# Performance work log

Measured on AMD Instinct MI355X. Metric: run time of the kernel, lower is better.

Reference implementation:

```python
import jax, jax.numpy as jnp
import numpy as np

B, C, H, W = 1, 128, 48, 48
HC = 32                     # head_channel
NH = C // HC                # num heads = 4
K = 16                      # n_clusters
N = H * W                   # 2304
SCALE = HC ** 0.5
EPS = 1e-6


def setup_inputs() -> dict:
    key = jax.random.key(0)
    ks = jax.random.split(key, 20)
    s = 0.05  # weight init scale ~ xavier-ish for C=128
    def g(i, shape, sc=s):
        return jax.random.normal(ks[i], shape, dtype=jnp.float32) * sc
    return {
        'q_img': g(0, (B, C, H, W), 1.0),
        'k_img_map': g(1, (B, C, H, W), 1.0),
        'v_img_map': g(2, (B, C, H, W), 1.0),
        'pixel_coefficients': jax.random.uniform(ks[3], (B, N, N), dtype=jnp.float32),
        'labels': jax.random.randint(ks[4], (B, H, W), 0, K),
        # projections (stored as [in, out]; y = x @ w + b)
        'wq': g(5, (C, C)), 'bq': jnp.zeros((C,), jnp.float32),
        'wk': g(6, (C, C)), 'bk': jnp.zeros((C,), jnp.float32),
        'wv': g(7, (C, C)), 'bv': jnp.zeros((C,), jnp.float32),
        # mlp_1: Linear(C,2C) -> LeakyReLU(0.01) -> Linear(2C,C) (dropout=0 -> identity)
        'w1a': g(8, (C, 2 * C)), 'b1a': jnp.zeros((2 * C,), jnp.float32),
        'w1b': g(9, (2 * C, C)), 'b1b': jnp.zeros((C,), jnp.float32),
        # mlp_2
        'w2a': g(10, (C, 2 * C)), 'b2a': jnp.zeros((2 * C,), jnp.float32),
        'w2b': g(11, (2 * C, C)), 'b2b': jnp.zeros((C,), jnp.float32),
    }


def _mlp(x, wa, ba, wb, bb):
    h = x @ wa + ba
    h = jax.nn.leaky_relu(h, negative_slope=0.01)
    return h @ wb + bb


def reference(q_img, k_img_map, v_img_map, pixel_coefficients,
              wq, bq, wk, bk, wv, bv,
              w1a, b1a, w1b, b1b, w2a, b2a, w2b, b2b,
              labels):
    # projections on channel-last pixels
    q = q_img.transpose(0, 2, 3, 1).reshape(B, N, C) @ wq + bq
    k = k_img_map.transpose(0, 2, 3, 1).reshape(B, N, C) @ wk + bk
    v = v_img_map.transpose(0, 2, 3, 1).reshape(B, N, C) @ wv + bv

    labels_flat = labels.reshape(B, N)
    onehot = jax.nn.one_hot(labels_flat, K, dtype=q.dtype)        # [B,N,K]
    num_k = jnp.einsum('bnk,bnc->bkc', onehot, k)                 # [B,K,C]
    den_k = onehot.sum(axis=1)[:, :, None] + EPS                  # [B,K,1]
    centers_k = num_k / den_k

    qm = q.reshape(B, N, NH, HC).transpose(0, 2, 1, 3)            # [B,h,N,d]
    km = k.reshape(B, N, NH, HC).transpose(0, 2, 1, 3)
    vm = v.reshape(B, N, NH, HC).transpose(0, 2, 1, 3)
    kcm = centers_k.reshape(B, K, NH, HC).transpose(0, 2, 1, 3)   # [B,h,K,d]

    attn_intra = jnp.einsum('bhid,bhjd->bhij', qm, km)            # [B,h,N,N]
    attn_centers = jnp.einsum('bhid,bhkd->bhik', qm, kcm)         # [B,h,N,K]

    # gather center score per key's cluster: attn_centers[b,h,i,labels[b,j]]
    idx = jnp.broadcast_to(labels_flat[:, None, None, :], (B, NH, N, N))
    attn_inter = jnp.take_along_axis(attn_centers, idx, axis=3)   # [B,h,N,N]
    attn_inter = attn_inter * pixel_coefficients[:, None, :, :]

    same = labels_flat[:, None, :, None] == labels_flat[:, None, None, :]  # [B,1,N,N]
    scores = jnp.where(same, attn_intra, attn_inter) / SCALE
    attn_w = jax.nn.softmax(scores, axis=-1)

    out = jnp.einsum('bhij,bhjd->bhid', attn_w, vm)
    out = out.transpose(0, 2, 1, 3).reshape(B, N, C)              # [B,N,C]

    v_spatial = v.reshape(B, H, W, C).transpose(0, 3, 1, 2)       # [B,C,H,W]
    rs1 = v_spatial + _mlp(out, w1a, b1a, w1b, b1b).transpose(0, 2, 1).reshape(B, C, H, W)
    rs1_flat = rs1.transpose(0, 2, 3, 1).reshape(B, N, C)
    rs2 = rs1 + _mlp(rs1_flat, w2a, b2a, w2b, b2b).transpose(0, 2, 1).reshape(B, C, H, W)
    return rs2
```

## Files before the change

### kernel.cpp

```cpp
#include <hip/hip_runtime.h>
#include <hip/hip_bf16.h>
#include <math.h>

#define NPIX 2304
#define CCH  128
#define NH   4
#define HC   32
#define NCL  16
#define KSPLIT 8
#define KEYS 288
#define NSTEP 9
#define QSCALE 0.25503489f
#define PPT  16

typedef __attribute__((ext_vector_type(8))) short short8;
typedef __attribute__((ext_vector_type(4))) float f32x4;

#if __has_builtin(__builtin_amdgcn_exp2f)
#define EXP2(x) __builtin_amdgcn_exp2f(x)
#else
#define EXP2(x) __expf((x) * 0.6931471805599453f)
#endif

static __device__ __forceinline__ short f2bf(float x) {
    __hip_bfloat16 b = __float2bfloat16(x);
    return *reinterpret_cast<short*>(&b);
}

__global__ void __launch_bounds__(256) pack_w_kernel(
        const float* __restrict__ w1a, const float* __restrict__ w1b,
        const float* __restrict__ w2a, const float* __restrict__ w2b,
        const float* __restrict__ wq,  const float* __restrict__ wk,
        const float* __restrict__ wv,
        float4* __restrict__ p1a, float4* __restrict__ p1b,
        float4* __restrict__ p2a, float4* __restrict__ p2b,
        float4* __restrict__ pq,  float4* __restrict__ pk,
        float4* __restrict__ pv) {
    const int idx = blockIdx.x * 256 + threadIdx.x;
    const float* src; float4* dst; int sh, local;
    if (idx < 8192)       { src = w1a; dst = p1a; sh = 8; local = idx; }
    else if (idx < 16384) { src = w1b; dst = p1b; sh = 7; local = idx - 8192; }
    else if (idx < 24576) { src = w2a; dst = p2a; sh = 8; local = idx - 16384; }
    else if (idx < 32768) { src = w2b; dst = p2b; sh = 7; local = idx - 24576; }
    else if (idx < 36864) { src = wq;  dst = pq;  sh = 7; local = idx - 32768; }
    else if (idx < 40960) { src = wk;  dst = pk;  sh = 7; local = idx - 36864; }
    else                  { src = wv;  dst = pv;  sh = 7; local = idx - 40960; }
    const int OUT = 1 << sh;
    const int g = local >> sh, o = local & (OUT - 1);
    float4 v;
    v.x = src[(4 * g + 0) * OUT + o];
    v.y = src[(4 * g + 1) * OUT + o];
    v.z = src[(4 * g + 2) * OUT + o];
    v.w = src[(4 * g + 3) * OUT + o];
    dst[local] = v;
}

__global__ void __launch_bounds__(256) proj_kernel(
        const float* __restrict__ xq, const float* __restrict__ xk,
        const float* __restrict__ xv, const int* __restrict__ labels,
        const float4* __restrict__ pq, const float* __restrict__ bq,
        const float4* __restrict__ pk, const float* __restrict__ bk,
        const float4* __restrict__ pv, const float* __restrict__ bv,
        short* __restrict__ qbf, short* __restrict__ kbf,
        float* __restrict__ vbuf, short* __restrict__ vbfT,
        float* __restrict__ cpart, float* __restrict__ denpart) {
    __shared__ float xsP[CCH * PPT];
    __shared__ float ls2[2 * NCL * CCH];
    __shared__ float smls[32];
    const int which = blockIdx.y;
    const int pxblk = blockIdx.x;
    const int n0    = pxblk * PPT;
    const int t  = threadIdx.x;
    const int c  = t & 127;
    const int ph = t >> 7;
    const float*  x  = (which == 0) ? xq : (which == 1) ? xk : xv;
    const float4* wp = (which == 0) ? pq : (which == 1) ? pk : pv;
    const float*  b  = (which == 0) ? bq : (which == 1) ? bk : bv;

#pragma unroll
    for (int it = 0; it < 8; ++it) {
        const int flat = it * 256 + t;
        const int cc = flat >> 4;
        const int p  = flat & 15;
        xsP[flat] = x[cc * NPIX + n0 + p];
    }
    if (which == 1)
        for (int u = t; u < 2 * NCL * CCH; u += 256) ls2[u] = 0.f;
    __syncthreads();

    float acc[8];
    const float bb = b[c];
#pragma unroll
    for (int p = 0; p < 8; ++p) acc[p] = bb;

    for (int g = 0; g < CCH / 4; ++g) {
        const float4 w4 = wp[g * 128 + c];
#pragma unroll
        for (int j = 0; j < 4; ++j) {
            const float wv_ = (j == 0) ? w4.x : (j == 1) ? w4.y : (j == 2) ? w4.z : w4.w;
            const float4 xa = *(const float4*)(xsP + (4 * g + j) * PPT + ph * 8);
            const float4 xb = *(const float4*)(xsP + (4 * g + j) * PPT + ph * 8 + 4);
            acc[0] = fmaf(xa.x, wv_, acc[0]); acc[1] = fmaf(xa.y, wv_, acc[1]);
            acc[2] = fmaf(xa.z, wv_, acc[2]); acc[3] = fmaf(xa.w, wv_, acc[3]);
            acc[4] = fmaf(xb.x, wv_, acc[4]); acc[5] = fmaf(xb.y, wv_, acc[5]);
            acc[6] = fmaf(xb.z, wv_, acc[6]); acc[7] = fmaf(xb.w, wv_, acc[7]);
        }
    }

    const int nb = n0 + ph * 8;
    if (which == 0) {
#pragma unroll
        for (int p = 0; p < 8; ++p)
            qbf[(size_t)(nb + p) * CCH + c] = f2bf(acc[p] * QSCALE);
    } else if (which == 1) {
#pragma unroll
        for (int p = 0; p < 8; ++p)
            kbf[(size_t)(nb + p) * CCH + c] = f2bf(acc[p]);
        int lab8[8];
#pragma unroll
        for (int p = 0; p < 8; ++p) lab8[p] = labels[nb + p];
#pragma unroll
        for (int p = 0; p < 8; ++p)
            ls2[(ph * NCL + lab8[p]) * CCH + c] += acc[p];
        if (t < 32) {
            const int g2 = t >> 4, cl = t & 15;
            int cnt = 0;
#pragma unroll
            for (int p = 0; p < 8; ++p)
                cnt += (labels[n0 + g2 * 8 + p] == cl) ? 1 : 0;
            smls[t] = (float)cnt;
        }
        __syncthreads();
        for (int u = t; u < NCL * CCH; u += 256)
            cpart[(size_t)pxblk * 2048 + u] = ls2[u] + ls2[2048 + u];
        if (t < 16)
            denpart[pxblk * 16 + t] = smls[t] + smls[16 + t];
    } else {
#pragma unroll
        for (int p = 0; p < 8; ++p) vbuf[(size_t)(nb + p) * CCH + c] = acc[p];
        short8 s0;
#pragma unroll
        for (int p = 0; p < 8; ++p) s0[p] = f2bf(acc[p]);
        *(short8*)(vbfT + (size_t)c * NPIX + nb) = s0;
    }
}

__global__ void centersB_kernel(const float* __restrict__ cpart,
                                const float* __restrict__ denpart,
                                short* __restrict__ cbf) {
    const int idx = blockIdx.x * 256 + threadIdx.x;
    const int kk  = idx >> 7;
    float den = 0.f, s = 0.f;
    for (int b = 0; b < 144; ++b) den += denpart[b * 16 + kk];
    for (int b = 0; b < 144; ++b) s   += cpart[(size_t)b * 2048 + idx];
    cbf[idx] = f2bf(s / (den + 1e-6f));
}

__global__ void __launch_bounds__(256, 4) attn_part_kernel(
        const short* __restrict__ qbf,  const short* __restrict__ kbf,
        const short* __restrict__ vbfT, const short* __restrict__ cbf,
        const int* __restrict__ labels, const float* __restrict__ pc,
        float* __restrict__ part_o, float* __restrict__ part_l) {
    __shared__ __align__(16) short Pl[NH][16 * 40];
    __shared__ __align__(16) float aclT[NH][16][16];
    __shared__ int   labl[KEYS];
    const int qt   = blockIdx.x;
    const int ks   = blockIdx.y;
    const int tid  = threadIdx.x;
    const int w    = tid >> 6;
    const int lane = tid & 63;
    const int quad = lane >> 4;
    const int lq   = lane & 15;
    const int i0   = qt * 16;
    const int j0   = ks * KEYS;

    for (int u = tid; u < KEYS / 4; u += 256)
        *(int4*)(labl + u * 4) = *(const int4*)(labels + j0 + u * 4);

    const short8 aq = *(const short8*)(qbf + (size_t)(i0 + lq) * CCH + w * HC + quad * 8);
    {
        const short8 bc = *(const short8*)(cbf + (size_t)lq * CCH + w * HC + quad * 8);
        f32x4 z = {0.f, 0.f, 0.f, 0.f};
        f32x4 acd = __builtin_amdgcn_mfma_f32_16x16x32_bf16(aq, bc, z, 0, 0, 0);
        *(f32x4*)(&aclT[w][lq][quad * 4]) = acd;
    }
    int labi[4];
#pragma unroll
    for (int r = 0; r < 4; ++r) labi[r] = labels[i0 + quad * 4 + r];

    __syncthreads();

    const short* kp  = kbf  + (size_t)(j0 + lq) * CCH + w * HC + quad * 8;
    const short* vp  = vbfT + (size_t)(w * HC + lq) * NPIX + j0 + quad * 8;
    const float* pcp = pc   + (size_t)(i0 + quad * 4) * NPIX + j0 + lq;

    short8 k0A, k1A, v0A, v1A, k0B, k1B, v0B, v1B;
    float pcA[8], pcB[8];
    f32x4 accO0 = {0.f, 0.f, 0.f, 0.f};
    f32x4 accO1 = {0.f, 0.f, 0.f, 0.f};
    float lp[4] = {0.f, 0.f, 0.f, 0.f};

#define ISSUE(K0_, K1_, V0_, V1_, s) do {                                         \
        K0_ = *(const short8*)(kp + (size_t)(s) * 32 * CCH);                      \
        K1_ = *(const short8*)(kp + (size_t)((s) * 32 + 16) * CCH);               \
        V0_ = *(const short8*)(vp + (s) * 32);                                    \
        V1_ = *(const short8*)(vp + (size_t)16 * NPIX + (s) * 32);                \
    } while (0)

#define ISSUE_PC(dst, s) do {                                                     \
        _Pragma("unroll")                                                         \
        for (int r_ = 0; r_ < 4; ++r_) {                                          \
            dst[r_ * 2 + 0] = pcp[(size_t)r_ * NPIX + (s) * 32];                  \
            dst[r_ * 2 + 1] = pcp[(size_t)r_ * NPIX + (s) * 32 + 16];             \
        }                                                                         \
    } while (0)

#define COMPUTE(s, K0_, K1_, V0_, V1_, PCUSE) do {                                \
        _Pragma("unroll")                                                         \
        for (int kh = 0; kh < 2; ++kh) {                                          \
            const short8 bk = (kh == 0) ? K0_ : K1_;                              \
            f32x4 z = {0.f, 0.f, 0.f, 0.f};                                       \
            const f32x4 sv = __builtin_amdgcn_mfma_f32_16x16x32_bf16(aq, bk, z, 0, 0, 0);\
            const int slab = labl[(s) * 32 + kh * 16 + lq];                       \
            const f32x4 av4 = *(const f32x4*)(&aclT[w][slab][quad * 4]);          \
            _Pragma("unroll")                                                     \
            for (int r = 0; r < 4; ++r) {                                         \
                const float sc_ = (slab == labi[r]) ? sv[r] : av4[r] * PCUSE[r * 2 + kh];\
                const float p   = EXP2(sc_);                                      \
                lp[r] += p;                                                       \
                Pl[w][(quad * 4 + r) * 40 + kh * 16 + lq] = f2bf(p);              \
            }                                                                     \
        }                                                                         \
        const short8 ap = *(const short8*)(&Pl[w][lq * 40 + quad * 8]);           \
        accO0 = __builtin_amdgcn_mfma_f32_16x16x32_bf16(ap, V0_, accO0, 0, 0, 0); \
        accO1 = __builtin_amdgcn_mfma_f32_16x16x32_bf16(ap, V1_, accO1, 0, 0, 0); \
    } while (0)

    ISSUE(k0A, k1A, v0A, v1A, 0);
    ISSUE_PC(pcA, 0);
    for (int sb = 0; sb < NSTEP; sb += 2) {
        if (sb + 1 < NSTEP) { ISSUE(k0B, k1B, v0B, v1B, sb + 1); ISSUE_PC(pcB, sb + 1); }
        COMPUTE(sb, k0A, k1A, v0A, v1A, pcA);
        if (sb + 1 < NSTEP) {
            if (sb + 2 < NSTEP) { ISSUE(k0A, k1A, v0A, v1A, sb + 2); ISSUE_PC(pcA, sb + 2); }
            COMPUTE(sb + 1, k0B, k1B, v0B, v1B, pcB);
        }
    }
#undef ISSUE
#undef ISSUE_PC
#undef COMPUTE

#pragma unroll
    for (int r = 0; r < 4; ++r) {
        float v = lp[r];
        v += __shfl_xor(v, 1, 64);
        v += __shfl_xor(v, 2, 64);
        v += __shfl_xor(v, 4, 64);
        v += __shfl_xor(v, 8, 64);
        lp[r] = v;
    }
    if (lq == 0) {
#pragma unroll
        for (int r = 0; r < 4; ++r)
            part_l[((size_t)ks * NPIX + i0 + quad * 4 + r) * NH + w] = lp[r];
    }
#pragma unroll
    for (int r = 0; r < 4; ++r) {
        float* po = part_o + ((size_t)ks * NPIX + i0 + quad * 4 + r) * CCH + w * HC;
        po[lq]      = accO0[r];
        po[16 + lq] = accO1[r];
    }
}

__global__ void __launch_bounds__(256) mlp_chain_kernel(
        const float* __restrict__ part_o, const float* __restrict__ part_l,
        const float* __restrict__ vbuf,
        const float4* __restrict__ p1a, const float* __restrict__ b1a,
        const float4* __restrict__ p1b, const float* __restrict__ b1b,
        const float4* __restrict__ p2a, const float* __restrict__ b2a,
        const float4* __restrict__ p2b, const float* __restrict__ b2b,
        float* __restrict__ outp) {
    __shared__ float xs[8 * CCH];
    __shared__ float hL[8 * 2 * CCH];
    __shared__ float r1L[8 * CCH];
    __shared__ float fT[CCH * 8];
    const int n0 = blockIdx.x * 8;
    const int t  = threadIdx.x;

    {
        const int p = t >> 5, c4 = (t & 31) * 4;
        const int hh2 = c4 >> 5;
        float ls_ = 0.f;
#pragma unroll
        for (int ks = 0; ks < KSPLIT; ++ks)
            ls_ += part_l[((size_t)ks * NPIX + n0 + p) * NH + hh2];
        float sx = 0.f, sy = 0.f, sz = 0.f, sw2 = 0.f;
#pragma unroll
        for (int ks = 0; ks < KSPLIT; ++ks) {
            const float4 v = *(const float4*)(part_o + ((size_t)ks * NPIX + n0 + p) * CCH + c4);
            sx += v.x; sy += v.y; sz += v.z; sw2 += v.w;
        }
        const float inv = 1.f / ls_;
        xs[p * CCH + c4 + 0] = sx * inv;
        xs[p * CCH + c4 + 1] = sy * inv;
        xs[p * CCH + c4 + 2] = sz * inv;
        xs[p * CCH + c4 + 3] = sw2 * inv;
    }
    __syncthreads();

    const int c  = t & 127;
    const int pg = t >> 7;

    {
        float ha[8];
        const float b1 = b1a[t];
#pragma unroll
        for (int p = 0; p < 8; ++p) ha[p] = b1;
        for (int g = 0; g < CCH / 4; ++g) {
            const float4 w4 = p1a[g * 2 * CCH + t];
#pragma unroll
            for (int p = 0; p < 8; ++p) {
                const float4 xv = *(const float4*)(xs + p * CCH + g * 4);
                ha[p] = fmaf(xv.x, w4.x, ha[p]); ha[p] = fmaf(xv.y, w4.y, ha[p]);
                ha[p] = fmaf(xv.z, w4.z, ha[p]); ha[p] = fmaf(xv.w, w4.w, ha[p]);
            }
        }
#pragma unroll
        for (int p = 0; p < 8; ++p) {
            const float v = ha[p];
            hL[p * 2 * CCH + t] = (v > 0.f) ? v : 0.01f * v;
        }
    }
    __syncthreads();

    {
        float oa[4];
        const float bo = b1b[c];
#pragma unroll
        for (int j = 0; j < 4; ++j) oa[j] = bo;
        for (int g = 0; g < 2 * CCH / 4; ++g) {
            const float4 w4 = p1b[g * CCH + c];
#pragma unroll
            for (int j = 0; j < 4; ++j) {
                const float4 hv = *(const float4*)(hL + (pg * 4 + j) * 2 * CCH + g * 4);
                oa[j] = fmaf(hv.x, w4.x, oa[j]); oa[j] = fmaf(hv.y, w4.y, oa[j]);
                oa[j] = fmaf(hv.z, w4.z, oa[j]); oa[j] = fmaf(hv.w, w4.w, oa[j]);
            }
        }
#pragma unroll
        for (int j = 0; j < 4; ++j)
            r1L[(pg * 4 + j) * CCH + c] =
                vbuf[(size_t)(n0 + pg * 4 + j) * CCH + c] + oa[j];
    }
    __syncthreads();

    {
        float ha[8];
        const float b2 = b2a[t];
#pragma unroll
        for (int p = 0; p < 8; ++p) ha[p] = b2;
        for (int g = 0; g < CCH / 4; ++g) {
            const float4 w4 = p2a[g * 2 * CCH + t];
#pragma unroll
            for (int p = 0; p < 8; ++p) {
                const float4 xv = *(const float4*)(r1L + p * CCH + g * 4);
                ha[p] = fmaf(xv.x, w4.x, ha[p]); ha[p] = fmaf(xv.y, w4.y, ha[p]);
                ha[p] = fmaf(xv.z, w4.z, ha[p]); ha[p] = fmaf(xv.w, w4.w, ha[p]);
            }
        }
        __syncthreads();
#pragma unroll
        for (int p = 0; p < 8; ++p) {
            const float v = ha[p];
            hL[p * 2 * CCH + t] = (v > 0.f) ? v : 0.01f * v;
        }
    }
    __syncthreads();

    {
        float oa[4];
        const float bo = b2b[c];
#pragma unroll
        for (int j = 0; j < 4; ++j) oa[j] = bo;
        for (int g = 0; g < 2 * CCH / 4; ++g) {
            const float4 w4 = p2b[g * CCH + c];
#pragma unroll
            for (int j = 0; j < 4; ++j) {
                const float4 hv = *(const float4*)(hL + (pg * 4 + j) * 2 * CCH + g * 4);
                oa[j] = fmaf(hv.x, w4.x, oa[j]); oa[j] = fmaf(hv.y, w4.y, oa[j]);
                oa[j] = fmaf(hv.z, w4.z, oa[j]); oa[j] = fmaf(hv.w, w4.w, oa[j]);
            }
        }
#pragma unroll
        for (int j = 0; j < 4; ++j)
            fT[c * 8 + pg * 4 + j] = r1L[(pg * 4 + j) * CCH + c] + oa[j];
    }
    __syncthreads();

    {
        const int cc = t >> 1, half = t & 1;
        const float4 v = *(const float4*)(fT + cc * 8 + half * 4);
        *(float4*)(outp + (size_t)cc * NPIX + n0 + half * 4) = v;
    }
}

extern "C" void kernel_launch(void* const* d_in, const int* in_sizes, int n_in,
                              void* d_out, int out_size, void* d_ws, size_t ws_size,
                              hipStream_t stream) {
    const float* q_img = (const float*)d_in[0];
    const float* k_img = (const float*)d_in[1];
    const float* v_img = (const float*)d_in[2];
    const float* pc    = (const float*)d_in[3];
    const int*   labels= (const int*)  d_in[4];
    const float* wq = (const float*)d_in[5];   const float* bq = (const float*)d_in[6];
    const float* wk = (const float*)d_in[7];   const float* bk = (const float*)d_in[8];
    const float* wv = (const float*)d_in[9];   const float* bv = (const float*)d_in[10];
    const float* w1a = (const float*)d_in[11]; const float* b1a = (const float*)d_in[12];
    const float* w1b = (const float*)d_in[13]; const float* b1b = (const float*)d_in[14];
    const float* w2a = (const float*)d_in[15]; const float* b2a = (const float*)d_in[16];
    const float* w2b = (const float*)d_in[17]; const float* b2b = (const float*)d_in[18];

    float* fw = (float*)d_ws;
    float* vbuf    = fw;
    float* part_o  = vbuf + (size_t)NPIX * CCH;
    float* part_l  = part_o + (size_t)KSPLIT * NPIX * CCH;
    float* cpart   = part_l + (size_t)KSPLIT * NPIX * NH;
    float* denpart = cpart + (size_t)144 * 2048;
    float* pkd     = denpart + 144 * 16;
    float4* p1a = (float4*)pkd;
    float4* p1b = p1a + 8192;
    float4* p2a = p1b + 8192;
    float4* p2b = p2a + 8192;
    float4* pq  = p2b + 8192;
    float4* pk4 = pq + 4096;
    float4* pv4 = pk4 + 4096;
    short* qbf     = (short*)(pv4 + 4096);
    short* kbf     = qbf + (size_t)NPIX * CCH;
    short* vbfT    = kbf + (size_t)NPIX * CCH;
    short* cbf     = vbfT + (size_t)NPIX * CCH;

    pack_w_kernel<<<176, 256, 0, stream>>>(
        w1a, w1b, w2a, w2b, wq, wk, wv, p1a, p1b, p2a, p2b, pq, pk4, pv4);
    proj_kernel<<<dim3(144, 3), 256, 0, stream>>>(
        q_img, k_img, v_img, labels, pq, bq, pk4, bk, pv4, bv,
        qbf, kbf, vbuf, vbfT, cpart, denpart);
    centersB_kernel<<<8, 256, 0, stream>>>(cpart, denpart, cbf);
    attn_part_kernel<<<dim3(144, KSPLIT), 256, 0, stream>>>(
        qbf, kbf, vbfT, cbf, labels, pc, part_o, part_l);
    mlp_chain_kernel<<<288, 256, 0, stream>>>(
        part_o, part_l, vbuf, p1a, b1a, p1b, b1b, p2a, b2a, p2b, b2b,
        (float*)d_out);
}
```

Before: 185.8 us.

## Run MLP chain on bf16 MFMA with transposed bf16 weight packing

Replaces the scalar-FMA fp32 MLP chain with bf16 MFMA 16x16x32 tiles, processing 16 pixels per block instead of 8. The pack kernel now emits transposed bf16 copies of the four MLP weight matrices laid out for MFMA B operands. Intermediate activations are staged in padded bf16 shared memory, while the residual is kept in fp32 registers. This cuts ALU time in the MLP stage, at the cost of bf16 rounding in the MLP inputs and weights and a halved block count.

```diff
diff --git a/kernel.cpp b/kernel.cpp
--- a/kernel.cpp
+++ b/kernel.cpp
@@ -14,6 +14,7 @@
 #define PPT  16
 
 typedef __attribute__((ext_vector_type(8))) short short8;
+typedef __attribute__((ext_vector_type(4))) short short4v;
 typedef __attribute__((ext_vector_type(4))) float f32x4;
 
 #if __has_builtin(__builtin_amdgcn_exp2f)
@@ -28,31 +29,46 @@
 }
 
 __global__ void __launch_bounds__(256) pack_w_kernel(
+        const float* __restrict__ wq,  const float* __restrict__ wk,
+        const float* __restrict__ wv,
         const float* __restrict__ w1a, const float* __restrict__ w1b,
         const float* __restrict__ w2a, const float* __restrict__ w2b,
-        const float* __restrict__ wq,  const float* __restrict__ wk,
-        const float* __restrict__ wv,
-        float4* __restrict__ p1a, float4* __restrict__ p1b,
-        float4* __restrict__ p2a, float4* __restrict__ p2b,
         float4* __restrict__ pq,  float4* __restrict__ pk,
-        float4* __restrict__ pv) {
+        float4* __restrict__ pv,
+        short* __restrict__ t1a, short* __restrict__ t1b,
+        short* __restrict__ t2a, short* __restrict__ t2b) {
     const int idx = blockIdx.x * 256 + threadIdx.x;
-    const float* src; float4* dst; int sh, local;
-    if (idx < 8192)       { src = w1a; dst = p1a; sh = 8; local = idx; }
-    else if (idx < 16384) { src = w1b; dst = p1b; sh = 7; local = idx - 8192; }
-    else if (idx < 24576) { src = w2a; dst = p2a; sh = 8; local = idx - 16384; }
-    else if (idx < 32768) { src = w2b; dst = p2b; sh = 7; local = idx - 24576; }
-    else if (idx < 36864) { src = wq;  dst = pq;  sh = 7; local = idx - 32768; }
-    else if (idx < 40960) { src = wk;  dst = pk;  sh = 7; local = idx - 36864; }
-    else                  { src = wv;  dst = pv;  sh = 7; local = idx - 40960; }
-    const int OUT = 1 << sh;
-    const int g = local >> sh, o = local & (OUT - 1);
-    float4 v;
-    v.x = src[(4 * g + 0) * OUT + o];
-    v.y = src[(4 * g + 1) * OUT + o];
-    v.z = src[(4 * g + 2) * OUT + o];
-    v.w = src[(4 * g + 3) * OUT + o];
-    dst[local] = v;
+    if (idx < 12288) {
+        const int which = idx >> 12, local = idx & 4095;
+        const float* src = (which == 0) ? wq : (which == 1) ? wk : wv;
+        float4*      dst = (which == 0) ? pq : (which == 1) ? pk : pv;
+        const int g = local >> 7, o = local & 127;
+        float4 v;
+        v.x = src[(4 * g + 0) * 128 + o];
+        v.y = src[(4 * g + 1) * 128 + o];
+        v.z = src[(4 * g + 2) * 128 + o];
+        v.w = src[(4 * g + 3) * 128 + o];
+        dst[local] = v;
+    } else {
+        const int i2 = idx - 12288;
+        const int which = i2 >> 12, local = i2 & 4095;
+        short8 s;
+        if (which == 0 || which == 2) {
+            const float* src = (which == 0) ? w1a : w2a;
+            short*       dst = (which == 0) ? t1a : t2a;
+            const int o = local >> 4, g = local & 15;
+#pragma unroll
+            for (int j = 0; j < 8; ++j) s[j] = f2bf(src[(g * 8 + j) * 256 + o]);
+            *(short8*)(dst + (size_t)o * 128 + g * 8) = s;
+        } else {
+            const float* src = (which == 1) ? w1b : w2b;
+            short*       dst = (which == 1) ? t1b : t2b;
+            const int o = local >> 5, g = local & 31;
+#pragma unroll
+            for (int j = 0; j < 8; ++j) s[j] = f2bf(src[(g * 8 + j) * 128 + o]);
+            *(short8*)(dst + (size_t)o * 256 + g * 8) = s;
+        }
+    }
 }
 
 __global__ void __launch_bounds__(256) proj_kernel(
@@ -272,28 +288,30 @@
     }
 }
 
-__global__ void __launch_bounds__(256) mlp_chain_kernel(
+#define XS 136
+#define HS 264
+__global__ void __launch_bounds__(256) mlp_mfma_kernel(
         const float* __restrict__ part_o, const float* __restrict__ part_l,
         const float* __restrict__ vbuf,
-        const float4* __restrict__ p1a, const float* __restrict__ b1a,
-        const float4* __restrict__ p1b, const float* __restrict__ b1b,
-        const float4* __restrict__ p2a, const float* __restrict__ b2a,
-        const float4* __restrict__ p2b, const float* __restrict__ b2b,
+        const short* __restrict__ t1a, const float* __restrict__ b1a,
+        const short* __restrict__ t1b, const float* __restrict__ b1b,
+        const short* __restrict__ t2a, const float* __restrict__ b2a,
+        const short* __restrict__ t2b, const float* __restrict__ b2b,
         float* __restrict__ outp) {
-    __shared__ float xs[8 * CCH];
-    __shared__ float hL[8 * 2 * CCH];
-    __shared__ float r1L[8 * CCH];
-    __shared__ float fT[CCH * 8];
-    const int n0 = blockIdx.x * 8;
+    __shared__ __align__(16) short xbf[16 * XS];
+    __shared__ __align__(16) short hbf[16 * HS];
+    __shared__ __align__(16) short r1bf[16 * XS];
+    __shared__ float fT[128 * 20];
+    const int n0 = blockIdx.x * 16;
     const int t  = threadIdx.x;
-
-    {
-        const int p = t >> 5, c4 = (t & 31) * 4;
-        const int hh2 = c4 >> 5;
+    const int w  = t >> 6, lane = t & 63, quad = lane >> 4, lq = lane & 15;
+
+    for (int u = t; u < 512; u += 256) {
+        const int p = u >> 5, c4 = (u & 31) * 4, hh = c4 >> 5;
         float ls_ = 0.f;
 #pragma unroll
         for (int ks = 0; ks < KSPLIT; ++ks)
-            ls_ += part_l[((size_t)ks * NPIX + n0 + p) * NH + hh2];
+            ls_ += part_l[((size_t)ks * NPIX + n0 + p) * NH + hh];
         float sx = 0.f, sy = 0.f, sz = 0.f, sw2 = 0.f;
 #pragma unroll
         for (int ks = 0; ks < KSPLIT; ++ks) {
@@ -301,106 +319,116 @@
             sx += v.x; sy += v.y; sz += v.z; sw2 += v.w;
         }
         const float inv = 1.f / ls_;
-        xs[p * CCH + c4 + 0] = sx * inv;
-        xs[p * CCH + c4 + 1] = sy * inv;
-        xs[p * CCH + c4 + 2] = sz * inv;
-        xs[p * CCH + c4 + 3] = sw2 * inv;
-    }
-    __syncthreads();
-
-    const int c  = t & 127;
-    const int pg = t >> 7;
+        short4v s;
+        s[0] = f2bf(sx * inv); s[1] = f2bf(sy * inv);
+        s[2] = f2bf(sz * inv); s[3] = f2bf(sw2 * inv);
+        *(short4v*)(xbf + p * XS + c4) = s;
+    }
+    __syncthreads();
 
     {
-        float ha[8];
-        const float b1 = b1a[t];
-#pragma unroll
-        for (int p = 0; p < 8; ++p) ha[p] = b1;
-        for (int g = 0; g < CCH / 4; ++g) {
-            const float4 w4 = p1a[g * 2 * CCH + t];
-#pragma unroll
-            for (int p = 0; p < 8; ++p) {
-                const float4 xv = *(const float4*)(xs + p * CCH + g * 4);
-                ha[p] = fmaf(xv.x, w4.x, ha[p]); ha[p] = fmaf(xv.y, w4.y, ha[p]);
-                ha[p] = fmaf(xv.z, w4.z, ha[p]); ha[p] = fmaf(xv.w, w4.w, ha[p]);
-            }
-        }
-#pragma unroll
-        for (int p = 0; p < 8; ++p) {
-            const float v = ha[p];
-            hL[p * 2 * CCH + t] = (v > 0.f) ? v : 0.01f * v;
-        }
-    }
-    __syncthreads();
-
+        short8 a[4];
+#pragma unroll
+        for (int ks = 0; ks < 4; ++ks)
+            a[ks] = *(const short8*)(xbf + lq * XS + ks * 32 + quad * 8);
+#pragma unroll
+        for (int tile = 0; tile < 4; ++tile) {
+            const int out0 = w * 64 + tile * 16;
+            f32x4 acc = {0.f, 0.f, 0.f, 0.f};
+#pragma unroll
+            for (int ks = 0; ks < 4; ++ks) {
+                const short8 b = *(const short8*)(t1a + (size_t)(out0 + lq) * 128 + ks * 32 + quad * 8);
+                acc = __builtin_amdgcn_mfma_f32_16x16x32_bf16(a[ks], b, acc, 0, 0, 0);
+            }
+            const float bb = b1a[out0 + lq];
+#pragma unroll
+            for (int r = 0; r < 4; ++r) {
+                float v = acc[r] + bb;
+                v = (v > 0.f) ? v : 0.01f * v;
+                hbf[(quad * 4 + r) * HS + out0 + lq] = f2bf(v);
+            }
+        }
+    }
+    __syncthreads();
+
+    float rs1f[2][4];
     {
-        float oa[4];
-        const float bo = b1b[c];
-#pragma unroll
-        for (int j = 0; j < 4; ++j) oa[j] = bo;
-        for (int g = 0; g < 2 * CCH / 4; ++g) {
-            const float4 w4 = p1b[g * CCH + c];
-#pragma unroll
-            for (int j = 0; j < 4; ++j) {
-                const float4 hv = *(const float4*)(hL + (pg * 4 + j) * 2 * CCH + g * 4);
-                oa[j] = fmaf(hv.x, w4.x, oa[j]); oa[j] = fmaf(hv.y, w4.y, oa[j]);
-                oa[j] = fmaf(hv.z, w4.z, oa[j]); oa[j] = fmaf(hv.w, w4.w, oa[j]);
-            }
-        }
-#pragma unroll
-        for (int j = 0; j < 4; ++j)
-            r1L[(pg * 4 + j) * CCH + c] =
-                vbuf[(size_t)(n0 + pg * 4 + j) * CCH + c] + oa[j];
+        short8 a[8];
+#pragma unroll
+        for (int ks = 0; ks < 8; ++ks)
+            a[ks] = *(const short8*)(hbf + lq * HS + ks * 32 + quad * 8);
+#pragma unroll
+        for (int tile = 0; tile < 2; ++tile) {
+            const int out0 = w * 32 + tile * 16;
+            f32x4 acc = {0.f, 0.f, 0.f, 0.f};
+#pragma unroll
+            for (int ks = 0; ks < 8; ++ks) {
+                const short8 b = *(const short8*)(t1b + (size_t)(out0 + lq) * 256 + ks * 32 + quad * 8);
+                acc = __builtin_amdgcn_mfma_f32_16x16x32_bf16(a[ks], b, acc, 0, 0, 0);
+            }
+            const float bb = b1b[out0 + lq];
+#pragma unroll
+            for (int r = 0; r < 4; ++r) {
+                const float v = acc[r] + bb +
+                    vbuf[(size_t)(n0 + quad * 4 + r) * CCH + out0 + lq];
+                rs1f[tile][r] = v;
+                r1bf[(quad * 4 + r) * XS + out0 + lq] = f2bf(v);
+            }
+        }
     }
     __syncthreads();
 
     {
-        float ha[8];
-        const float b2 = b2a[t];
-#pragma unroll
-        for (int p = 0; p < 8; ++p) ha[p] = b2;
-        for (int g = 0; g < CCH / 4; ++g) {
-            const float4 w4 = p2a[g * 2 * CCH + t];
-#pragma unroll
-            for (int p = 0; p < 8; ++p) {
-                const float4 xv = *(const float4*)(r1L + p * CCH + g * 4);
-                ha[p] = fmaf(xv.x, w4.x, ha[p]); ha[p] = fmaf(xv.y, w4.y, ha[p]);
-                ha[p] = fmaf(xv.z, w4.z, ha[p]); ha[p] = fmaf(xv.w, w4.w, ha[p]);
-            }
-        }
-        __syncthreads();
-#pragma unroll
-        for (int p = 0; p < 8; ++p) {
-            const float v = ha[p];
-            hL[p * 2 * CCH + t] = (v > 0.f) ? v : 0.01f * v;
+        short8 a[4];
+#pragma unroll
+        for (int ks = 0; ks < 4; ++ks)
+            a[ks] = *(const short8*)(r1bf + lq * XS + ks * 32 + quad * 8);
+#pragma unroll
+        for (int tile = 0; tile < 4; ++tile) {
+            const int out0 = w * 64 + tile * 16;
+            f32x4 acc = {0.f, 0.f, 0.f, 0.f};
+#pragma unroll
+            for (int ks = 0; ks < 4; ++ks) {
+                const short8 b = *(const short8*)(t2a + (size_t)(out0 + lq) * 128 + ks * 32 + quad * 8);
+                acc = __builtin_amdgcn_mfma_f32_16x16x32_bf16(a[ks], b, acc, 0, 0, 0);
+            }
+            const float bb = b2a[out0 + lq];
+#pragma unroll
+            for (int r = 0; r < 4; ++r) {
+                float v = acc[r] + bb;
+                v = (v > 0.f) ? v : 0.01f * v;
+                hbf[(quad * 4 + r) * HS + out0 + lq] = f2bf(v);
+            }
         }
     }
     __syncthreads();
 
     {
-        float oa[4];
-        const float bo = b2b[c];
-#pragma unroll
-        for (int j = 0; j < 4; ++j) oa[j] = bo;
-        for (int g = 0; g < 2 * CCH / 4; ++g) {
-            const float4 w4 = p2b[g * CCH + c];
-#pragma unroll
-            for (int j = 0; j < 4; ++j) {
-                const float4 hv = *(const float4*)(hL + (pg * 4 + j) * 2 * CCH + g * 4);
-                oa[j] = fmaf(hv.x, w4.x, oa[j]); oa[j] = fmaf(hv.y, w4.y, oa[j]);
-                oa[j] = fmaf(hv.z, w4.z, oa[j]); oa[j] = fmaf(hv.w, w4.w, oa[j]);
-            }
-        }
-#pragma unroll
-        for (int j = 0; j < 4; ++j)
-            fT[c * 8 + pg * 4 + j] = r1L[(pg * 4 + j) * CCH + c] + oa[j];
-    }
-    __syncthreads();
-
-    {
-        const int cc = t >> 1, half = t & 1;
-        const float4 v = *(const float4*)(fT + cc * 8 + half * 4);
-        *(float4*)(outp + (size_t)cc * NPIX + n0 + half * 4) = v;
+        short8 a[8];
+#pragma unroll
+        for (int ks = 0; ks < 8; ++ks)
+            a[ks] = *(const short8*)(hbf + lq * HS + ks * 32 + quad * 8);
+#pragma unroll
+        for (int tile = 0; tile < 2; ++tile) {
+            const int out0 = w * 32 + tile * 16;
+            f32x4 acc = {0.f, 0.f, 0.f, 0.f};
+#pragma unroll
+            for (int ks = 0; ks < 8; ++ks) {
+                const short8 b = *(const short8*)(t2b + (size_t)(out0 + lq) * 256 + ks * 32 + quad * 8);
+                acc = __builtin_amdgcn_mfma_f32_16x16x32_bf16(a[ks], b, acc, 0, 0, 0);
+            }
+            const float bb = b2b[out0 + lq];
+#pragma unroll
+            for (int r = 0; r < 4; ++r)
+                fT[(out0 + lq) * 20 + quad * 4 + r] = acc[r] + bb + rs1f[tile][r];
+        }
+    }
+    __syncthreads();
+
+    for (int u = t; u < 512; u += 256) {
+        const int row = u >> 2, seg = u & 3;
+        const float4 v = *(const float4*)(fT + row * 20 + seg * 4);
+        *(float4*)(outp + (size_t)row * NPIX + n0 + seg * 4) = v;
     }
 }
 
@@ -426,28 +454,27 @@
     float* part_l  = part_o + (size_t)KSPLIT * NPIX * CCH;
     float* cpart   = part_l + (size_t)KSPLIT * NPIX * NH;
     float* denpart = cpart + (size_t)144 * 2048;
-    float* pkd     = denpart + 144 * 16;
-    float4* p1a = (float4*)pkd;
-    float4* p1b = p1a + 8192;
-    float4* p2a = p1b + 8192;
-    float4* p2b = p2a + 8192;
-    float4* pq  = p2b + 8192;
+    float4* pq  = (float4*)(denpart + 144 * 16);
     float4* pk4 = pq + 4096;
     float4* pv4 = pk4 + 4096;
-    short* qbf     = (short*)(pv4 + 4096);
-    short* kbf     = qbf + (size_t)NPIX * CCH;
-    short* vbfT    = kbf + (size_t)NPIX * CCH;
-    short* cbf     = vbfT + (size_t)NPIX * CCH;
-
-    pack_w_kernel<<<176, 256, 0, stream>>>(
-        w1a, w1b, w2a, w2b, wq, wk, wv, p1a, p1b, p2a, p2b, pq, pk4, pv4);
+    short* t1a  = (short*)(pv4 + 4096);
+    short* t1b  = t1a + 32768;
+    short* t2a  = t1b + 32768;
+    short* t2b  = t2a + 32768;
+    short* qbf  = t2b + 32768;
+    short* kbf  = qbf + (size_t)NPIX * CCH;
+    short* vbfT = kbf + (size_t)NPIX * CCH;
+    short* cbf  = vbfT + (size_t)NPIX * CCH;
+
+    pack_w_kernel<<<112, 256, 0, stream>>>(
+        wq, wk, wv, w1a, w1b, w2a, w2b, pq, pk4, pv4, t1a, t1b, t2a, t2b);
     proj_kernel<<<dim3(144, 3), 256, 0, stream>>>(
         q_img, k_img, v_img, labels, pq, bq, pk4, bk, pv4, bv,
         qbf, kbf, vbuf, vbfT, cpart, denpart);
     centersB_kernel<<<8, 256, 0, stream>>>(cpart, denpart, cbf);
     attn_part_kernel<<<dim3(144, KSPLIT), 256, 0, stream>>>(
         qbf, kbf, vbfT, cbf, labels, pc, part_o, part_l);
-    mlp_chain_kernel<<<288, 256, 0, stream>>>(
-        part_o, part_l, vbuf, p1a, b1a, p1b, b1b, p2a, b2a, p2b, b2b,
+    mlp_mfma_kernel<<<144, 256, 0, stream>>>(
+        part_o, part_l, vbuf, t1a, b1a, t1b, b1b, t2a, b2a, t2b, b2b,
         (float*)d_out);
 }
```

Measured after the change: 157.5 us. 15.2% less time.
